# Performance work log

Measured on AMD Instinct MI355X. Metric: run time of the kernel, lower is better.

Reference implementation:

```python
import jax, jax.numpy as jnp
import numpy as np
from jax import lax

IN_FEATURES = 8192
OUT_FEATURES = 28672


def _unpack3(qweight, infeatures):
    """Unpack GPTQ-style 3-bit weights.

    qweight: (infeatures//32*3, O) int32. Every 3 consecutive int32 rows hold
    32 packed 3-bit values per column (GPTQ quant.py packing): values 0-9 in
    word0 bits [0..30), value 10 split over word0[30:32]|word1[0:1],
    values 11-20 in word1 bits [1..31), value 21 split over word1[31:32]|word2[0:2],
    values 22-31 in word2 bits [2..32).
    Returns float32 (infeatures, O) with raw quant codes in [0, 8).
    """
    O = qweight.shape[1]
    G = infeatures // 32
    q = lax.bitcast_convert_type(qweight, jnp.uint32).reshape(G, 3, O)
    w0, w1, w2 = q[:, 0], q[:, 1], q[:, 2]
    sh = jnp.arange(10, dtype=jnp.uint32)  # 10 whole values per word
    v0 = (w0[:, None, :] >> (3 * sh)[None, :, None]) & 7          # (G,10,O)
    v10 = (((w0 >> 30) & 3) | ((w1 & 1) << 2))[:, None, :]        # (G,1,O)
    v1 = (w1[:, None, :] >> (3 * sh + 1)[None, :, None]) & 7       # (G,10,O)
    v21 = (((w1 >> 31) & 1) | ((w2 & 3) << 1))[:, None, :]        # (G,1,O)
    v2 = (w2[:, None, :] >> (3 * sh + 2)[None, :, None]) & 7       # (G,10,O)
    vals = jnp.concatenate([v0, v10, v1, v21, v2], axis=1)        # (G,32,O)
    return vals.reshape(infeatures, O).astype(jnp.float32)


def setup_inputs() -> dict:
    key = jax.random.key(0)
    k1, k2, k3, k4, k5 = jax.random.split(key, 5)
    x = jax.random.normal(k1, (1, IN_FEATURES), dtype=jnp.float32)
    qweight = jax.random.randint(k2, (IN_FEATURES // 32 * 3, OUT_FEATURES), 0, 2147483647, dtype=jnp.int32)
    scales = jax.random.uniform(k3, (OUT_FEATURES, 1), dtype=jnp.float32)
    zeros = jax.random.normal(k4, (OUT_FEATURES, 1), dtype=jnp.float32)
    bias = jax.random.normal(k5, (OUT_FEATURES,), dtype=jnp.float32)
    return {"x": x, "qweight": qweight, "scales": scales, "zeros": zeros, "bias": bias}


def reference(x, qweight, scales, zeros, bias):
    infeatures = x.shape[-1]
    q = _unpack3(qweight, infeatures)            # (K, O) float codes
    # per-output-channel dequant: W[k, o] = scales[o] * q[k, o] - zeros[o]
    W = scales.T * q - zeros.T                   # (K, O)
    y = x @ W + bias                             # (1, O)
    return y
```

## Files before the change

kernel.cpp:

```cpp
#include <hip/hip_runtime.h>
#include <stdint.h>


constexpr int O_FEAT  = 28672;
constexpr int IN_FEAT = 8192;
constexpr int NGROUP  = IN_FEAT / 32;
constexpr int SPLIT   = 32;
constexpr int GPB     = NGROUP / SPLIT;
constexpr int O4      = O_FEAT / 4;

typedef uint32_t uint32x4 __attribute__((ext_vector_type(4)));
typedef float    floatx4  __attribute__((ext_vector_type(4)));

__device__ __forceinline__ void dot_group(uint32_t w0, uint32_t w1, uint32_t w2,
                                          const float xv[32], float& acc) {
  float a0 = acc, a1 = 0.f, a2 = 0.f;
  #pragma unroll
  for (int j = 0; j < 10; ++j) a0 += xv[j] * (float)((w0 >> (3 * j)) & 7u);
  a0 += xv[10] * (float)((w0 >> 30) | ((w1 & 1u) << 2));
  #pragma unroll
  for (int j = 0; j < 10; ++j) a1 += xv[11 + j] * (float)((w1 >> (3 * j + 1)) & 7u);
  a1 += xv[21] * (float)((w1 >> 31) | ((w2 & 3u) << 1));
  #pragma unroll
  for (int j = 0; j < 10; ++j) a2 += xv[22 + j] * (float)((w2 >> (3 * j + 2)) & 7u);
  acc = a0 + (a1 + a2);
}

__global__ __launch_bounds__(128) void q3_partial(const float* __restrict__ x,
                                                  const uint32x4* __restrict__ qw4,
                                                  floatx4* __restrict__ part) {
  const int tcol4 = blockIdx.x * 128 + threadIdx.x;
  const int g0    = blockIdx.y * GPB;
  const uint32x4* qp = qw4 + (size_t)(3 * g0) * O4 + tcol4;
  const float*    xp = x + g0 * 32;
  float acc0 = 0.f, acc1 = 0.f, acc2 = 0.f, acc3 = 0.f;

  uint32x4 wa = qp[0];
  uint32x4 wb = qp[O4];
  uint32x4 wc = qp[2 * O4];

  #pragma unroll
  for (int g = 0; g < GPB; ++g) {
    uint32x4 na = {0, 0, 0, 0}, nb = {0, 0, 0, 0}, nc = {0, 0, 0, 0};
    qp += 3 * O4;
    if (g < GPB - 1) {
      na = qp[0];
      nb = qp[O4];
      nc = qp[2 * O4];
    }

    float xv[32];
    const float4* x4 = reinterpret_cast<const float4*>(xp);
    #pragma unroll
    for (int u = 0; u < 8; ++u) {
      float4 t = x4[u];
      xv[4 * u + 0] = t.x; xv[4 * u + 1] = t.y;
      xv[4 * u + 2] = t.z; xv[4 * u + 3] = t.w;
    }
    xp += 32;

    dot_group(wa.x, wb.x, wc.x, xv, acc0);
    dot_group(wa.y, wb.y, wc.y, xv, acc1);
    dot_group(wa.z, wb.z, wc.z, xv, acc2);
    dot_group(wa.w, wb.w, wc.w, xv, acc3);

    wa = na; wb = nb; wc = nc;
  }

  floatx4 r = {acc0, acc1, acc2, acc3};
  part[(size_t)blockIdx.y * O4 + tcol4] = r;
}

__global__ __launch_bounds__(256) void q3_finish(const float* __restrict__ x,
                                                 const float* __restrict__ part,
                                                 const float* __restrict__ scales,
                                                 const float* __restrict__ zeros,
                                                 const float* __restrict__ bias,
                                                 float* __restrict__ out) {
  float s = 0.f;
  const float4* x4 = reinterpret_cast<const float4*>(x);
  for (int i = threadIdx.x; i < IN_FEAT / 4; i += 256) {
    float4 t = x4[i];
    s += (t.x + t.y) + (t.z + t.w);
  }
  #pragma unroll
  for (int off = 32; off > 0; off >>= 1) s += __shfl_down(s, off, 64);
  __shared__ float ls[4];
  if ((threadIdx.x & 63) == 0) ls[threadIdx.x >> 6] = s;
  __syncthreads();
  float S = (ls[0] + ls[1]) + (ls[2] + ls[3]);

  int o = blockIdx.x * 256 + threadIdx.x;
  float sum = 0.f;
  #pragma unroll
  for (int y = 0; y < SPLIT; ++y) sum += part[(size_t)y * O_FEAT + o];
  out[o] = scales[o] * sum - zeros[o] * S + bias[o];
}

extern "C" void kernel_launch(void* const* d_in, const int* in_sizes, int n_in,
                              void* d_out, int out_size, void* d_ws, size_t ws_size,
                              hipStream_t stream) {
  const float*    x      = (const float*)d_in[0];
  const uint32x4* qw4    = (const uint32x4*)d_in[1];
  const float*    scales = (const float*)d_in[2];
  const float*    zeros  = (const float*)d_in[3];
  const float*    bias   = (const float*)d_in[4];
  float*          out    = (float*)d_out;
  floatx4*        part   = (floatx4*)d_ws;

  q3_partial<<<dim3(O4 / 128, SPLIT), dim3(128), 0, stream>>>(x, qw4, part);
  q3_finish<<<dim3(O_FEAT / 256), dim3(256), 0, stream>>>(x, (const float*)part,
                                                          scales, zeros, bias, out);
}
```

Measured before the change: 145.3 us.

## Fuse split-K reduction and dequant epilogue into partial kernel via atomics

Removes the separate finish kernel and the partial-sum workspace. Each block now computes its chunk's sum of x, applies scales, zeros and bias (bias only for the first split) and atomically adds four outputs into a zeroed output buffer. This saves a kernel launch and the 3.6MB partial write and read, but adds a memset plus 32-way float atomic contention per output and makes the summation order nondeterministic.

```diff
diff --git a/kernel.cpp b/kernel.cpp
--- a/kernel.cpp
+++ b/kernel.cpp
@@ -10,7 +10,6 @@
 constexpr int O4      = O_FEAT / 4;
 
 typedef uint32_t uint32x4 __attribute__((ext_vector_type(4)));
-typedef float    floatx4  __attribute__((ext_vector_type(4)));
 
 __device__ __forceinline__ void dot_group(uint32_t w0, uint32_t w1, uint32_t w2,
                                           const float xv[32], float& acc) {
@@ -26,13 +25,25 @@
   acc = a0 + (a1 + a2);
 }
 
-__global__ __launch_bounds__(128) void q3_partial(const float* __restrict__ x,
-                                                  const uint32x4* __restrict__ qw4,
-                                                  floatx4* __restrict__ part) {
+__global__ __launch_bounds__(128) void q3_fused(const float* __restrict__ x,
+                                                const uint32x4* __restrict__ qw4,
+                                                const float* __restrict__ scales,
+                                                const float* __restrict__ zeros,
+                                                const float* __restrict__ bias,
+                                                float* __restrict__ out) {
   const int tcol4 = blockIdx.x * 128 + threadIdx.x;
   const int g0    = blockIdx.y * GPB;
   const uint32x4* qp = qw4 + (size_t)(3 * g0) * O4 + tcol4;
   const float*    xp = x + g0 * 32;
+
+  float sc = xp[threadIdx.x * 2] + xp[threadIdx.x * 2 + 1];
+  #pragma unroll
+  for (int off = 32; off > 0; off >>= 1) sc += __shfl_down(sc, off, 64);
+  __shared__ float ls[2];
+  if ((threadIdx.x & 63) == 0) ls[threadIdx.x >> 6] = sc;
+  __syncthreads();
+  const float S_chunk = ls[0] + ls[1];
+
   float acc0 = 0.f, acc1 = 0.f, acc2 = 0.f, acc3 = 0.f;
 
   uint32x4 wa = qp[0];
@@ -67,34 +78,21 @@
     wa = na; wb = nb; wc = nc;
   }
 
-  floatx4 r = {acc0, acc1, acc2, acc3};
-  part[(size_t)blockIdx.y * O4 + tcol4] = r;
-}
-
-__global__ __launch_bounds__(256) void q3_finish(const float* __restrict__ x,
-                                                 const float* __restrict__ part,
-                                                 const float* __restrict__ scales,
-                                                 const float* __restrict__ zeros,
-                                                 const float* __restrict__ bias,
-                                                 float* __restrict__ out) {
-  float s = 0.f;
-  const float4* x4 = reinterpret_cast<const float4*>(x);
-  for (int i = threadIdx.x; i < IN_FEAT / 4; i += 256) {
-    float4 t = x4[i];
-    s += (t.x + t.y) + (t.z + t.w);
+  const float4 sv = reinterpret_cast<const float4*>(scales)[tcol4];
+  const float4 zv = reinterpret_cast<const float4*>(zeros)[tcol4];
+  float c0 = sv.x * acc0 - zv.x * S_chunk;
+  float c1 = sv.y * acc1 - zv.y * S_chunk;
+  float c2 = sv.z * acc2 - zv.z * S_chunk;
+  float c3 = sv.w * acc3 - zv.w * S_chunk;
+  if (blockIdx.y == 0) {
+    const float4 bv = reinterpret_cast<const float4*>(bias)[tcol4];
+    c0 += bv.x; c1 += bv.y; c2 += bv.z; c3 += bv.w;
   }
-  #pragma unroll
-  for (int off = 32; off > 0; off >>= 1) s += __shfl_down(s, off, 64);
-  __shared__ float ls[4];
-  if ((threadIdx.x & 63) == 0) ls[threadIdx.x >> 6] = s;
-  __syncthreads();
-  float S = (ls[0] + ls[1]) + (ls[2] + ls[3]);
-
-  int o = blockIdx.x * 256 + threadIdx.x;
-  float sum = 0.f;
-  #pragma unroll
-  for (int y = 0; y < SPLIT; ++y) sum += part[(size_t)y * O_FEAT + o];
-  out[o] = scales[o] * sum - zeros[o] * S + bias[o];
+  float* op = out + 4 * (size_t)tcol4;
+  atomicAdd(op + 0, c0);
+  atomicAdd(op + 1, c1);
+  atomicAdd(op + 2, c2);
+  atomicAdd(op + 3, c3);
 }
 
 extern "C" void kernel_launch(void* const* d_in, const int* in_sizes, int n_in,
@@ -106,9 +104,8 @@
   const float*    zeros  = (const float*)d_in[3];
   const float*    bias   = (const float*)d_in[4];
   float*          out    = (float*)d_out;
-  floatx4*        part   = (floatx4*)d_ws;
 
-  q3_partial<<<dim3(O4 / 128, SPLIT), dim3(128), 0, stream>>>(x, qw4, part);
-  q3_finish<<<dim3(O_FEAT / 256), dim3(256), 0, stream>>>(x, (const float*)part,
-                                                          scales, zeros, bias, out);
+  hipMemsetAsync(out, 0, (size_t)out_size * sizeof(float), stream);
+  q3_fused<<<dim3(O4 / 128, SPLIT), dim3(128), 0, stream>>>(x, qw4, scales, zeros,
+                                                            bias, out);
 }
```

New measurement: 145.4 us. No clear change (+0.1%).
